# Kernel tuning notes

Hardware: AMD Instinct MI355X
Metric: run time of the kernel (lower is better)

The kernel has to match this reference:

```python
import jax, jax.numpy as jnp
import numpy as np
from jax import lax
from jax.scipy.special import logsumexp

NUM_STATES = 32
INPUT_SIZE = 128
HIDDEN = 256
LN_EPS = 1e-5


def setup_inputs() -> dict:
    key = jax.random.key(0)
    ks = jax.random.split(key, 8)
    B, T = 32, 8192
    x = jax.random.normal(ks[0], (B, T, INPUT_SIZE), dtype=jnp.float32)
    # parameters (match torch defaults: initial_logits=zeros, transition_logits=2*I)
    initial_logits = jnp.zeros((NUM_STATES,), jnp.float32)
    transition_logits = 2.0 * jnp.eye(NUM_STATES, dtype=jnp.float32)
    W1 = jax.random.normal(ks[1], (INPUT_SIZE, HIDDEN), jnp.float32) / np.sqrt(INPUT_SIZE)
    b1 = jnp.zeros((HIDDEN,), jnp.float32)
    ln_g = jnp.ones((HIDDEN,), jnp.float32)
    ln_b = jnp.zeros((HIDDEN,), jnp.float32)
    W2 = jax.random.normal(ks[2], (HIDDEN, HIDDEN), jnp.float32) / np.sqrt(HIDDEN)
    b2 = jnp.zeros((HIDDEN,), jnp.float32)
    W3 = jax.random.normal(ks[3], (HIDDEN, NUM_STATES), jnp.float32) / np.sqrt(HIDDEN)
    b3 = jnp.zeros((NUM_STATES,), jnp.float32)
    return {"x": x, "initial_logits": initial_logits, "transition_logits": transition_logits,
            "W1": W1, "b1": b1, "ln_g": ln_g, "ln_b": ln_b, "W2": W2, "b2": b2, "W3": W3, "b3": b3}


def _emission_logprobs(x, W1, b1, ln_g, ln_b, W2, b2, W3, b3):
    h = x @ W1 + b1                                   # (B,T,H)
    mu = h.mean(-1, keepdims=True)
    var = ((h - mu) ** 2).mean(-1, keepdims=True)
    h = (h - mu) * lax.rsqrt(var + LN_EPS) * ln_g + ln_b
    h = jax.nn.gelu(h, approximate=False)             # torch nn.GELU default = exact
    h = jax.nn.gelu(h @ W2 + b2, approximate=False)
    logits = h @ W3 + b3                              # (B,T,S)  (dropout inactive at eval)
    return jax.nn.log_softmax(logits, axis=-1)


def reference(x, initial_logits, transition_logits, W1, b1, ln_g, ln_b, W2, b2, W3, b3):
    emissions = _emission_logprobs(x, W1, b1, ln_g, ln_b, W2, b2, W3, b3)  # (B,T,S)
    B = x.shape[0]
    trans = jax.nn.softmax(transition_logits, axis=-1)
    log_trans = jnp.log(trans + 1e-10)                               # (S,S)
    log_init = jnp.log(jax.nn.softmax(initial_logits) + 1e-10)       # (S,)

    alpha0 = log_init[None, :] + emissions[:, 0, :]                  # (B,S)
    em_rest = jnp.swapaxes(emissions[:, 1:, :], 0, 1)                # (T-1,B,S)

    # --- forward algorithm (log-sum-exp semiring scan over time) ---
    def fwd_step(alpha, em_t):
        a = em_t + logsumexp(alpha[:, :, None] + log_trans[None, :, :], axis=1)
        return a, a
    _, alphas_rest = lax.scan(fwd_step, alpha0, em_rest)             # (T-1,B,S)
    alphas = jnp.concatenate([alpha0[:, None, :], jnp.swapaxes(alphas_rest, 0, 1)], axis=1)  # (B,T,S)
    log_likelihood = logsumexp(alphas[:, -1, :], axis=-1)            # (B,)
    state_probs = jax.nn.softmax(alphas, axis=-1)

    # --- Viterbi (max-plus semiring scan + backtrace) ---
    def vit_step(vit, em_t):
        scores = vit[:, :, None] + log_trans[None, :, :]             # (B,S,S)
        return scores.max(axis=1) + em_t, scores.argmax(axis=1)
    vit_last, bps = lax.scan(vit_step, alpha0, em_rest)              # bps: (T-1,B,S) int32
    path_score = vit_last.max(axis=-1)
    last_state = vit_last.argmax(axis=-1)                            # (B,)
    bidx = jnp.arange(B)

    def bt_step(state, bp):
        prev = bp[bidx, state]
        return prev, prev
    _, path_prefix = lax.scan(bt_step, last_state, bps, reverse=True)  # (T-1,B)
    best_path = jnp.concatenate([jnp.swapaxes(path_prefix, 0, 1), last_state[:, None]], axis=1)  # (B,T)

    return (emissions, state_probs, log_likelihood, trans, best_path, path_score)
```

## Files before the change

kernel.cpp:

```cpp
#include <hip/hip_runtime.h>
#include <cstdint>
#include <cstddef>

#define TT 8192
#define SS 32

__device__ __forceinline__ float rsum32(float v){
    v += __shfl_xor(v,16); v += __shfl_xor(v,8); v += __shfl_xor(v,4);
    v += __shfl_xor(v,2);  v += __shfl_xor(v,1); return v;
}
__device__ __forceinline__ float rmax32(float v){
    v = fmaxf(v,__shfl_xor(v,16)); v = fmaxf(v,__shfl_xor(v,8)); v = fmaxf(v,__shfl_xor(v,4));
    v = fmaxf(v,__shfl_xor(v,2));  v = fmaxf(v,__shfl_xor(v,1)); return v;
}
__device__ __forceinline__ void lds_read32(const float* p, float* d){
    #pragma unroll
    for (int k=0;k<8;k++){
        float4 v = ((const float4*)p)[k];
        d[4*k+0]=v.x; d[4*k+1]=v.y; d[4*k+2]=v.z; d[4*k+3]=v.w;
    }
}
__device__ __forceinline__ float arr_sum32(const float* a){
    float s0=0.f,s1=0.f,s2=0.f,s3=0.f;
    #pragma unroll
    for (int k=0;k<32;k+=4){ s0+=a[k]; s1+=a[k+1]; s2+=a[k+2]; s3+=a[k+3]; }
    return (s0+s1)+(s2+s3);
}
__device__ __forceinline__ float arr_max32(const float* a){
    float s0=a[0],s1=a[1],s2=a[2],s3=a[3];
    #pragma unroll
    for (int k=4;k<32;k+=4){ s0=fmaxf(s0,a[k]); s1=fmaxf(s1,a[k+1]); s2=fmaxf(s2,a[k+2]); s3=fmaxf(s3,a[k+3]); }
    return fmaxf(fmaxf(s0,s1),fmaxf(s2,s3));
}
__device__ __forceinline__ float dot32(const float* a, const float* b){
    float s0=0.f,s1=0.f,s2=0.f,s3=0.f;
    #pragma unroll
    for (int k=0;k<32;k+=4){
        s0=fmaf(a[k],b[k],s0); s1=fmaf(a[k+1],b[k+1],s1);
        s2=fmaf(a[k+2],b[k+2],s2); s3=fmaf(a[k+3],b[k+3],s3);
    }
    return (s0+s1)+(s2+s3);
}
__device__ __forceinline__ float gelu_exact(float v){
    return 0.5f*v*(1.0f + erff(v*0.70710678118654752440f));
}

__global__ __launch_bounds__(1024) void hmm_prep(
    const float* __restrict__ il, const float* __restrict__ tl,
    float* __restrict__ trans, float* __restrict__ lt, float* __restrict__ li,
    float* __restrict__ LL, float* __restrict__ PS)
{
    const int tid = threadIdx.x;
    const int c = tid & 31;
    const float v = tl[tid];
    const float m = rmax32(v);
    const float e = expf(v - m);
    const float ssum = rsum32(e);
    const float t = e / ssum;
    trans[tid] = t;
    lt[tid] = logf(t + 1e-10f);
    if (tid < 32){
        const float iv = il[c];
        const float m2 = rmax32(iv);
        const float e2 = expf(iv - m2);
        const float s2 = rsum32(e2);
        li[c] = logf(e2/s2 + 1e-10f);
        LL[c] = 0.f;
        PS[c] = 0.f;
    }
}

__global__ __launch_bounds__(256) void hmm_mlp(
    const float* __restrict__ x,
    const float* __restrict__ W1, const float* __restrict__ b1,
    const float* __restrict__ lng, const float* __restrict__ lnb,
    const float* __restrict__ W2, const float* __restrict__ b2,
    const float* __restrict__ W3, const float* __restrict__ b3,
    float* __restrict__ em_out)
{
    __shared__ float smem[16384];
    float* h1s = smem;
    float* xs  = smem + 8192;
    float* h2s = smem + 8192;

    const int tid = threadIdx.x;
    const int row0 = blockIdx.x << 5;

    {
        const float4* xg = (const float4*)(x + (size_t)row0*128);
        float4* xs4 = (float4*)xs;
        #pragma unroll
        for (int l=0;l<4;l++) xs4[tid + (l<<8)] = xg[tid + (l<<8)];
    }
    __syncthreads();

    const int tc_ = tid & 31;
    const int ty  = tid >> 5;
    const int c0  = tc_ << 3;
    const int r0g = ty << 2;

    float acc[4][8];
    #pragma unroll
    for (int i=0;i<4;i++){
        #pragma unroll
        for (int j=0;j<8;j++) acc[i][j]=0.f;
    }

    {
        const float4* W14 = (const float4*)W1;
        #pragma unroll 2
        for (int k4=0;k4<32;k4++){
            float xv[4][4];
            #pragma unroll
            for (int i=0;i<4;i++){
                float4 t = *(const float4*)&xs[(r0g+i)*128 + (k4<<2)];
                xv[i][0]=t.x; xv[i][1]=t.y; xv[i][2]=t.z; xv[i][3]=t.w;
            }
            #pragma unroll
            for (int kk=0;kk<4;kk++){
                const int k = (k4<<2)+kk;
                const float4 wa = W14[k*64 + (tc_<<1)];
                const float4 wb = W14[k*64 + (tc_<<1) + 1];
                const float w[8] = {wa.x,wa.y,wa.z,wa.w,wb.x,wb.y,wb.z,wb.w};
                #pragma unroll
                for (int i=0;i<4;i++){
                    #pragma unroll
                    for (int j=0;j<8;j++) acc[i][j] = fmaf(xv[i][kk], w[j], acc[i][j]);
                }
            }
        }
    }

    {
        float4 ta = *(const float4*)&b1[c0];  float4 tb = *(const float4*)&b1[c0+4];
        const float bb[8] = {ta.x,ta.y,ta.z,ta.w,tb.x,tb.y,tb.z,tb.w};
        ta = *(const float4*)&lng[c0]; tb = *(const float4*)&lng[c0+4];
        const float gg[8] = {ta.x,ta.y,ta.z,ta.w,tb.x,tb.y,tb.z,tb.w};
        ta = *(const float4*)&lnb[c0]; tb = *(const float4*)&lnb[c0+4];
        const float be[8] = {ta.x,ta.y,ta.z,ta.w,tb.x,tb.y,tb.z,tb.w};
        #pragma unroll
        for (int i=0;i<4;i++){
            float sm=0.f;
            #pragma unroll
            for (int j=0;j<8;j++){ float v = acc[i][j]+bb[j]; acc[i][j]=v; sm+=v; }
            float sq=0.f;
            #pragma unroll
            for (int j=0;j<8;j++) sq = fmaf(acc[i][j],acc[i][j],sq);
            sm = rsum32(sm); sq = rsum32(sq);
            const float mu = sm*(1.f/256.f);
            const float var = sq*(1.f/256.f) - mu*mu;
            const float rstd = rsqrtf(var + 1e-5f);
            #pragma unroll
            for (int j=0;j<8;j++){
                float v = (acc[i][j]-mu)*rstd*gg[j] + be[j];
                acc[i][j] = gelu_exact(v);
            }
            float4 s0 = make_float4(acc[i][0],acc[i][1],acc[i][2],acc[i][3]);
            float4 s1 = make_float4(acc[i][4],acc[i][5],acc[i][6],acc[i][7]);
            *(float4*)&h1s[(r0g+i)*256 + c0]     = s0;
            *(float4*)&h1s[(r0g+i)*256 + c0 + 4] = s1;
        }
    }
    __syncthreads();

    #pragma unroll
    for (int i=0;i<4;i++){
        #pragma unroll
        for (int j=0;j<8;j++) acc[i][j]=0.f;
    }
    {
        const float4* W24 = (const float4*)W2;
        #pragma unroll 2
        for (int k4=0;k4<64;k4++){
            float xv[4][4];
            #pragma unroll
            for (int i=0;i<4;i++){
                float4 t = *(const float4*)&h1s[(r0g+i)*256 + (k4<<2)];
                xv[i][0]=t.x; xv[i][1]=t.y; xv[i][2]=t.z; xv[i][3]=t.w;
            }
            #pragma unroll
            for (int kk=0;kk<4;kk++){
                const int k = (k4<<2)+kk;
                const float4 wa = W24[k*64 + (tc_<<1)];
                const float4 wb = W24[k*64 + (tc_<<1) + 1];
                const float w[8] = {wa.x,wa.y,wa.z,wa.w,wb.x,wb.y,wb.z,wb.w};
                #pragma unroll
                for (int i=0;i<4;i++){
                    #pragma unroll
                    for (int j=0;j<8;j++) acc[i][j] = fmaf(xv[i][kk], w[j], acc[i][j]);
                }
            }
        }
    }
    {
        float4 ta = *(const float4*)&b2[c0];  float4 tb = *(const float4*)&b2[c0+4];
        const float bb[8] = {ta.x,ta.y,ta.z,ta.w,tb.x,tb.y,tb.z,tb.w};
        #pragma unroll
        for (int i=0;i<4;i++){
            const int r = r0g + i;
            const int sw = (r & 7) << 2;
            #pragma unroll
            for (int j=0;j<8;j++) acc[i][j] = gelu_exact(acc[i][j]+bb[j]);
            float4 s0 = make_float4(acc[i][0],acc[i][1],acc[i][2],acc[i][3]);
            float4 s1 = make_float4(acc[i][4],acc[i][5],acc[i][6],acc[i][7]);
            *(float4*)&h2s[r*256 + (c0 ^ sw)]       = s0;
            *(float4*)&h2s[r*256 + ((c0+4) ^ sw)]   = s1;
        }
    }
    __syncthreads();

    {
        const int r3 = tid >> 3;
        const int cg = tid & 7;
        const int sw3 = (r3 & 7) << 2;
        float a3[4] = {0.f,0.f,0.f,0.f};
        const float4* W34 = (const float4*)W3;
        #pragma unroll 2
        for (int k4=0;k4<64;k4++){
            float4 hv = *(const float4*)&h2s[r3*256 + ((k4<<2) ^ sw3)];
            const float h[4] = {hv.x,hv.y,hv.z,hv.w};
            #pragma unroll
            for (int kk=0;kk<4;kk++){
                float4 w = W34[((k4<<2)+kk)*8 + cg];
                a3[0]=fmaf(h[kk],w.x,a3[0]); a3[1]=fmaf(h[kk],w.y,a3[1]);
                a3[2]=fmaf(h[kk],w.z,a3[2]); a3[3]=fmaf(h[kk],w.w,a3[3]);
            }
        }
        float4 b3v = ((const float4*)b3)[cg];
        a3[0]+=b3v.x; a3[1]+=b3v.y; a3[2]+=b3v.z; a3[3]+=b3v.w;
        float m = fmaxf(fmaxf(a3[0],a3[1]),fmaxf(a3[2],a3[3]));
        m = fmaxf(m,__shfl_xor(m,4)); m = fmaxf(m,__shfl_xor(m,2)); m = fmaxf(m,__shfl_xor(m,1));
        float se = expf(a3[0]-m)+expf(a3[1]-m)+expf(a3[2]-m)+expf(a3[3]-m);
        se += __shfl_xor(se,4); se += __shfl_xor(se,2); se += __shfl_xor(se,1);
        const float lz = m + logf(se);
        float4 o = make_float4(a3[0]-lz, a3[1]-lz, a3[2]-lz, a3[3]-lz);
        *(float4*)&em_out[((size_t)(row0+r3))*32 + (cg<<2)] = o;
    }
}

__global__ __launch_bounds__(256) void hmm_fwd(
    const float* __restrict__ em, const float* __restrict__ trans,
    const float* __restrict__ li, float* __restrict__ sp, float* __restrict__ LL)
{
    __shared__ float Ab[8][32];
    const int lane = threadIdx.x & 63;
    const int s = lane & 31;
    const int ci = ((threadIdx.x >> 6) << 1) | (lane >> 5);
    const int cid = (blockIdx.x << 3) + ci;
    const int b = cid >> 7;
    const int c = cid & 127;
    const int t0 = c << 6;

    float tc[32];
    #pragma unroll
    for (int k=0;k<32;k++) tc[k] = trans[(k<<5) + s];
    float* A = Ab[ci];
    const float* emb = em + (size_t)b*(TT*SS);
    const float li_s = li[s];

    A[s] = 0.03125f;
    asm volatile("s_waitcnt lgkmcnt(0)" ::: "memory");
    __builtin_amdgcn_wave_barrier();

    float sig = 0.f;
    float araw_prev = 0.f;

    const int tws = t0 - 64;
    float pe[8];
    #pragma unroll
    for (int j=0;j<8;j++){ int tt = tws + j; tt = tt < 0 ? 0 : tt; pe[j] = emb[(tt<<5) + s]; }

    #pragma unroll 1
    for (int g=0; g<8; g++){
        float ce[8];
        #pragma unroll
        for (int j=0;j<8;j++) ce[j] = pe[j];
        #pragma unroll
        for (int j=0;j<8;j++){ int tt = tws + ((g+1)<<3) + j; tt = tt < 0 ? 0 : tt; pe[j] = emb[(tt<<5) + s]; }
        #pragma unroll
        for (int j=0;j<8;j++){
            float Av[32];
            lds_read32(A, Av);
            const float sum = arr_sum32(Av);
            const float val = dot32(Av, tc);
            const float rs = 1.0f / sum;
            const float e = __expf(ce[j]);
            const float araw = val * rs * e;
            __builtin_amdgcn_wave_barrier();
            A[s] = araw;
            asm volatile("s_waitcnt lgkmcnt(0)" ::: "memory");
            __builtin_amdgcn_wave_barrier();
        }
    }

    #pragma unroll 1
    for (int g=0; g<8; g++){
        float ce[8];
        #pragma unroll
        for (int j=0;j<8;j++) ce[j] = pe[j];
        #pragma unroll
        for (int j=0;j<8;j++){ int tt = t0 + ((g+1)<<3) + j; tt = tt > (TT-1) ? (TT-1) : tt; pe[j] = emb[(tt<<5) + s]; }
        #pragma unroll
        for (int j=0;j<8;j++){
            const int i = (g<<3) + j;
            const int t = t0 + i;
            float Av[32];
            lds_read32(A, Av);
            const float sum = arr_sum32(Av);
            const float val = dot32(Av, tc);
            const float rs = 1.0f / sum;
            if (i > 0){
                sp[((size_t)b*TT + (t-1))*SS + s] = araw_prev * rs;
                sig += __logf(sum);
            }
            const float e = __expf(ce[j]);
            float araw = val * rs * e;
            if (c == 0 && i == 0) araw = __expf(li_s) * e;
            __builtin_amdgcn_wave_barrier();
            A[s] = araw;
            asm volatile("s_waitcnt lgkmcnt(0)" ::: "memory");
            __builtin_amdgcn_wave_barrier();
            araw_prev = araw;
        }
    }
    {
        float Av[32];
        lds_read32(A, Av);
        const float sum = arr_sum32(Av);
        const float rs = 1.0f / sum;
        sp[((size_t)b*TT + (t0+63))*SS + s] = araw_prev * rs;
        sig += __logf(sum);
    }
    if (s == 0) atomicAdd(&LL[b], sig);
}

__global__ __launch_bounds__(256) void hmm_vit(
    const float* __restrict__ em, const float* __restrict__ lt,
    const float* __restrict__ li, unsigned char* __restrict__ bps,
    float* __restrict__ PS, int* __restrict__ last_state)
{
    __shared__ float Vb[8][32];
    const int lane = threadIdx.x & 63;
    const int s = lane & 31;
    const int ci = ((threadIdx.x >> 6) << 1) | (lane >> 5);
    const int cid = (blockIdx.x << 3) + ci;
    const int b = cid >> 7;
    const int c = cid & 127;
    const int t0 = c << 6;

    float ltc[32];
    #pragma unroll
    for (int k=0;k<32;k++) ltc[k] = lt[(k<<5) + s];
    float* V = Vb[ci];
    const float* emb = em + (size_t)b*(TT*SS);
    const float li_s = li[s];

    V[s] = 0.f;
    asm volatile("s_waitcnt lgkmcnt(0)" ::: "memory");
    __builtin_amdgcn_wave_barrier();

    float delta = 0.f;

    const int tws = t0 - 128;
    float pe[8];
    #pragma unroll
    for (int j=0;j<8;j++){ int tt = tws + j; tt = tt < 0 ? 0 : tt; pe[j] = emb[(tt<<5) + s]; }

    #pragma unroll 1
    for (int g=0; g<16; g++){
        float ce[8];
        #pragma unroll
        for (int j=0;j<8;j++) ce[j] = pe[j];
        #pragma unroll
        for (int j=0;j<8;j++){ int tt = tws + ((g+1)<<3) + j; tt = tt < 0 ? 0 : tt; pe[j] = emb[(tt<<5) + s]; }
        #pragma unroll
        for (int j=0;j<8;j++){
            float Vv[32];
            lds_read32(V, Vv);
            float b0=-3.0e38f,b1v=-3.0e38f,b2v=-3.0e38f,b3v=-3.0e38f;
            #pragma unroll
            for (int k=0;k<32;k+=4){
                b0  = fmaxf(b0,  Vv[k]+ltc[k]);
                b1v = fmaxf(b1v, Vv[k+1]+ltc[k+1]);
                b2v = fmaxf(b2v, Vv[k+2]+ltc[k+2]);
                b3v = fmaxf(b3v, Vv[k+3]+ltc[k+3]);
            }
            float v = fmaxf(fmaxf(b0,b1v),fmaxf(b2v,b3v)) + ce[j];
            if (j == 7) v -= arr_max32(Vv);
            __builtin_amdgcn_wave_barrier();
            V[s] = v;
            asm volatile("s_waitcnt lgkmcnt(0)" ::: "memory");
            __builtin_amdgcn_wave_barrier();
        }
    }
    {
        float Vv[32];
        lds_read32(V, Vv);
        const float mm = arr_max32(Vv);
        __builtin_amdgcn_wave_barrier();
        V[s] = Vv[s] - mm;
        asm volatile("s_waitcnt lgkmcnt(0)" ::: "memory");
        __builtin_amdgcn_wave_barrier();
    }

    #pragma unroll 1
    for (int g=0; g<8; g++){
        float ce[8];
        #pragma unroll
        for (int j=0;j<8;j++) ce[j] = pe[j];
        #pragma unroll
        for (int j=0;j<8;j++){ int tt = t0 + ((g+1)<<3) + j; tt = tt > (TT-1) ? (TT-1) : tt; pe[j] = emb[(tt<<5) + s]; }
        #pragma unroll
        for (int j=0;j<8;j++){
            const int i = (g<<3) + j;
            const int t = t0 + i;
            float Vv[32];
            lds_read32(V, Vv);
            float B0=Vv[0]+ltc[0], B1=Vv[1]+ltc[1], B2=Vv[2]+ltc[2], B3=Vv[3]+ltc[3];
            int I0=0,I1=1,I2=2,I3=3;
            #pragma unroll
            for (int k=4;k<32;k+=4){
                float q0=Vv[k]+ltc[k];     if (q0>B0){B0=q0;I0=k;}
                float q1=Vv[k+1]+ltc[k+1]; if (q1>B1){B1=q1;I1=k+1;}
                float q2=Vv[k+2]+ltc[k+2]; if (q2>B2){B2=q2;I2=k+2;}
                float q3=Vv[k+3]+ltc[k+3]; if (q3>B3){B3=q3;I3=k+3;}
            }
            float best = B0; int bi = I0;
            if (B1>best || (B1==best && I1<bi)){best=B1;bi=I1;}
            if (B2>best || (B2==best && I2<bi)){best=B2;bi=I2;}
            if (B3>best || (B3==best && I3<bi)){best=B3;bi=I3;}
            float mmc = 0.f;
            if (j == 0){ mmc = arr_max32(Vv); delta += mmc; }
            float v;
            if (c == 0 && i == 0){
                v = li_s + ce[j];
            } else {
                v = best + ce[j] - mmc;
                bps[((size_t)b*TT + t)*SS + s] = (unsigned char)bi;
            }
            __builtin_amdgcn_wave_barrier();
            V[s] = v;
            asm volatile("s_waitcnt lgkmcnt(0)" ::: "memory");
            __builtin_amdgcn_wave_barrier();
        }
    }
    {
        float Vv[32];
        lds_read32(V, Vv);
        const float mm = arr_max32(Vv);
        delta += mm;
        if (c == 127){
            float best = Vv[0]; int bi = 0;
            #pragma unroll
            for (int k=1;k<32;k++){ if (Vv[k] > best){ best = Vv[k]; bi = k; } }
            if (s == 0) last_state[b] = bi;
        }
        if (s == 0) atomicAdd(&PS[b], delta);
    }
}

__global__ __launch_bounds__(64) void hmm_btc(
    const unsigned char* __restrict__ bps, unsigned char* __restrict__ pos,
    unsigned char* __restrict__ gmap)
{
    __shared__ unsigned char bp[8192];
    const int b = blockIdx.x >> 5;
    const int cb = blockIdx.x & 31;
    const int tbase = cb << 8;
    {
        const uint4* src = (const uint4*)(bps + ((size_t)b*TT + tbase)*SS);
        uint4* dst = (uint4*)bp;
        #pragma unroll
        for (int l=0;l<8;l++) dst[threadIdx.x + (l<<6)] = src[threadIdx.x + (l<<6)];
    }
    __syncthreads();
    if (threadIdx.x < 32){
        int cur = threadIdx.x;
        unsigned char* pc = pos + (((size_t)b<<5) + cb)*8192;
        #pragma unroll 1
        for (int t=255; t>=0; t--){
            pc[(t<<5) + threadIdx.x] = (unsigned char)cur;
            if ((tbase + t) >= 1) cur = bp[(t<<5) + cur];
        }
        gmap[(((b<<5) + cb)<<5) + threadIdx.x] = (unsigned char)cur;
    }
}

__global__ __launch_bounds__(256) void hmm_btb(
    const unsigned char* __restrict__ gmap, const int* __restrict__ last_state,
    unsigned char* __restrict__ e_tab)
{
    __shared__ unsigned char gl[32768];
    #pragma unroll
    for (int l=0;l<8;l++) ((uint4*)gl)[threadIdx.x + (l<<8)] = ((const uint4*)gmap)[threadIdx.x + (l<<8)];
    __syncthreads();
    if (threadIdx.x < 32){
        const int b = threadIdx.x;
        int s = last_state[b];
        #pragma unroll 1
        for (int cb=31; cb>=1; cb--){
            e_tab[(b<<5)+cb] = (unsigned char)s;
            s = gl[(((b<<5)+cb)<<5) + s];
        }
        e_tab[b<<5] = (unsigned char)s;
    }
}

__global__ __launch_bounds__(256) void hmm_btf(
    const unsigned char* __restrict__ pos, const unsigned char* __restrict__ e_tab,
    float* __restrict__ path)
{
    const int i = blockIdx.x*256 + threadIdx.x;
    const int b = i >> 13;
    const int t = i & (TT-1);
    const int cb = t >> 8;
    const int e = e_tab[(b<<5) + cb];
    const unsigned char v = pos[((((size_t)b<<5) + cb)<<13) + ((t & 255)<<5) + e];
    path[i] = (float)v;
}

extern "C" void kernel_launch(void* const* d_in, const int* in_sizes, int n_in,
                              void* d_out, int out_size, void* d_ws, size_t ws_size,
                              hipStream_t stream)
{
    const float* x   = (const float*)d_in[0];
    const float* il  = (const float*)d_in[1];
    const float* tl  = (const float*)d_in[2];
    const float* W1  = (const float*)d_in[3];
    const float* b1  = (const float*)d_in[4];
    const float* lng = (const float*)d_in[5];
    const float* lnb = (const float*)d_in[6];
    const float* W2  = (const float*)d_in[7];
    const float* b2  = (const float*)d_in[8];
    const float* W3  = (const float*)d_in[9];
    const float* b3  = (const float*)d_in[10];

    float* out   = (float*)d_out;
    float* em    = out;
    float* sp    = out + 8388608;
    float* LL    = out + 16777216;
    float* trans = out + 16777248;
    float* path  = out + 16778272;
    float* PS    = out + 17040416;

    char* wsb = (char*)d_ws;
    float* lt            = (float*)(wsb);
    float* li            = (float*)(wsb + 4096);
    int* last_state      = (int*)(wsb + 4224);
    unsigned char* e_tab = (unsigned char*)(wsb + 4352);
    unsigned char* bps   = (unsigned char*)(wsb + 8192);
    unsigned char* pos   = (unsigned char*)(wsb + 8192 + 8388608);
    unsigned char* gmap  = (unsigned char*)(wsb + 8192 + 16777216);

    hmm_prep<<<1, 1024, 0, stream>>>(il, tl, trans, lt, li, LL, PS);
    hmm_mlp<<<8192, 256, 0, stream>>>(x, W1, b1, lng, lnb, W2, b2, W3, b3, em);
    hmm_fwd<<<512, 256, 0, stream>>>(em, trans, li, sp, LL);
    hmm_vit<<<512, 256, 0, stream>>>(em, lt, li, bps, PS, last_state);
    hmm_btc<<<1024, 64, 0, stream>>>(bps, pos, gmap);
    hmm_btb<<<1, 256, 0, stream>>>(gmap, last_state, e_tab);
    hmm_btf<<<1024, 256, 0, stream>>>(pos, e_tab, path);
}
```

Baseline: 1.434 ms.

## Restructure MLP kernel so each wavefront owns rows, removing block barriers

The emission MLP is remapped so each 64-lane wavefront owns 8 rows and each lane owns 4 output columns. The x tile is no longer staged in LDS: x is read directly from global memory through a wave-uniform pointer, and the hidden activations reuse a single 32 KB LDS buffer in place. Since every wavefront only reads rows it wrote itself, all block-wide __syncthreads are dropped. LDS use is halved and launch_bounds asks for 5 blocks per CU to raise occupancy, at the cost of reading x from global per k-step and a tighter register budget.

```diff
diff --git a/kernel.cpp b/kernel.cpp
--- a/kernel.cpp
+++ b/kernel.cpp
@@ -12,6 +12,10 @@
 __device__ __forceinline__ float rmax32(float v){
     v = fmaxf(v,__shfl_xor(v,16)); v = fmaxf(v,__shfl_xor(v,8)); v = fmaxf(v,__shfl_xor(v,4));
     v = fmaxf(v,__shfl_xor(v,2));  v = fmaxf(v,__shfl_xor(v,1)); return v;
+}
+__device__ __forceinline__ float rsum64(float v){
+    v += __shfl_xor(v,32); v += __shfl_xor(v,16); v += __shfl_xor(v,8);
+    v += __shfl_xor(v,4);  v += __shfl_xor(v,2);  v += __shfl_xor(v,1); return v;
 }
 __device__ __forceinline__ void lds_read32(const float* p, float* d){
     #pragma unroll
@@ -70,7 +74,7 @@
     }
 }
 
-__global__ __launch_bounds__(256) void hmm_mlp(
+__global__ __launch_bounds__(256, 5) void hmm_mlp(
     const float* __restrict__ x,
     const float* __restrict__ W1, const float* __restrict__ b1,
     const float* __restrict__ lng, const float* __restrict__ lnb,
@@ -78,155 +82,114 @@
     const float* __restrict__ W3, const float* __restrict__ b3,
     float* __restrict__ em_out)
 {
-    __shared__ float smem[16384];
-    float* h1s = smem;
-    float* xs  = smem + 8192;
-    float* h2s = smem + 8192;
-
-    const int tid = threadIdx.x;
+    __shared__ float hbuf[8192];
+    const int tid  = threadIdx.x;
+    const int lane = tid & 63;
+    const int wv   = tid >> 6;
     const int row0 = blockIdx.x << 5;
-
-    {
-        const float4* xg = (const float4*)(x + (size_t)row0*128);
-        float4* xs4 = (float4*)xs;
-        #pragma unroll
-        for (int l=0;l<4;l++) xs4[tid + (l<<8)] = xg[tid + (l<<8)];
-    }
-    __syncthreads();
-
-    const int tc_ = tid & 31;
-    const int ty  = tid >> 5;
-    const int c0  = tc_ << 3;
-    const int r0g = ty << 2;
-
-    float acc[4][8];
-    #pragma unroll
-    for (int i=0;i<4;i++){
-        #pragma unroll
-        for (int j=0;j<8;j++) acc[i][j]=0.f;
-    }
-
-    {
-        const float4* W14 = (const float4*)W1;
-        #pragma unroll 2
-        for (int k4=0;k4<32;k4++){
-            float xv[4][4];
-            #pragma unroll
-            for (int i=0;i<4;i++){
-                float4 t = *(const float4*)&xs[(r0g+i)*128 + (k4<<2)];
-                xv[i][0]=t.x; xv[i][1]=t.y; xv[i][2]=t.z; xv[i][3]=t.w;
-            }
-            #pragma unroll
-            for (int kk=0;kk<4;kk++){
-                const int k = (k4<<2)+kk;
-                const float4 wa = W14[k*64 + (tc_<<1)];
-                const float4 wb = W14[k*64 + (tc_<<1) + 1];
-                const float w[8] = {wa.x,wa.y,wa.z,wa.w,wb.x,wb.y,wb.z,wb.w};
-                #pragma unroll
-                for (int i=0;i<4;i++){
-                    #pragma unroll
-                    for (int j=0;j<8;j++) acc[i][j] = fmaf(xv[i][kk], w[j], acc[i][j]);
-                }
-            }
-        }
-    }
-
-    {
-        float4 ta = *(const float4*)&b1[c0];  float4 tb = *(const float4*)&b1[c0+4];
-        const float bb[8] = {ta.x,ta.y,ta.z,ta.w,tb.x,tb.y,tb.z,tb.w};
-        ta = *(const float4*)&lng[c0]; tb = *(const float4*)&lng[c0+4];
-        const float gg[8] = {ta.x,ta.y,ta.z,ta.w,tb.x,tb.y,tb.z,tb.w};
-        ta = *(const float4*)&lnb[c0]; tb = *(const float4*)&lnb[c0+4];
-        const float be[8] = {ta.x,ta.y,ta.z,ta.w,tb.x,tb.y,tb.z,tb.w};
-        #pragma unroll
-        for (int i=0;i<4;i++){
-            float sm=0.f;
-            #pragma unroll
-            for (int j=0;j<8;j++){ float v = acc[i][j]+bb[j]; acc[i][j]=v; sm+=v; }
-            float sq=0.f;
-            #pragma unroll
-            for (int j=0;j<8;j++) sq = fmaf(acc[i][j],acc[i][j],sq);
-            sm = rsum32(sm); sq = rsum32(sq);
-            const float mu = sm*(1.f/256.f);
-            const float var = sq*(1.f/256.f) - mu*mu;
+    const int r0   = wv << 3;
+    const int c0   = lane << 2;
+
+    const int r0u = __builtin_amdgcn_readfirstlane(r0);
+    const float* xw = x + ((size_t)(row0 + r0u) << 7);
+
+    float acc[8][4];
+    #pragma unroll
+    for (int i=0;i<8;i++){ acc[i][0]=0.f; acc[i][1]=0.f; acc[i][2]=0.f; acc[i][3]=0.f; }
+
+    #pragma unroll 2
+    for (int k4=0;k4<32;k4++){
+        const float4 w0 = *(const float4*)&W1[((k4<<2)+0)*256 + c0];
+        const float4 w1 = *(const float4*)&W1[((k4<<2)+1)*256 + c0];
+        const float4 w2 = *(const float4*)&W1[((k4<<2)+2)*256 + c0];
+        const float4 w3 = *(const float4*)&W1[((k4<<2)+3)*256 + c0];
+        #pragma unroll
+        for (int i=0;i<8;i++){
+            const float4 xv = *(const float4*)(xw + (i<<7) + (k4<<2));
+            acc[i][0]=fmaf(xv.x,w0.x,acc[i][0]); acc[i][1]=fmaf(xv.x,w0.y,acc[i][1]);
+            acc[i][2]=fmaf(xv.x,w0.z,acc[i][2]); acc[i][3]=fmaf(xv.x,w0.w,acc[i][3]);
+            acc[i][0]=fmaf(xv.y,w1.x,acc[i][0]); acc[i][1]=fmaf(xv.y,w1.y,acc[i][1]);
+            acc[i][2]=fmaf(xv.y,w1.z,acc[i][2]); acc[i][3]=fmaf(xv.y,w1.w,acc[i][3]);
+            acc[i][0]=fmaf(xv.z,w2.x,acc[i][0]); acc[i][1]=fmaf(xv.z,w2.y,acc[i][1]);
+            acc[i][2]=fmaf(xv.z,w2.z,acc[i][2]); acc[i][3]=fmaf(xv.z,w2.w,acc[i][3]);
+            acc[i][0]=fmaf(xv.w,w3.x,acc[i][0]); acc[i][1]=fmaf(xv.w,w3.y,acc[i][1]);
+            acc[i][2]=fmaf(xv.w,w3.z,acc[i][2]); acc[i][3]=fmaf(xv.w,w3.w,acc[i][3]);
+        }
+    }
+
+    {
+        const float4 bb = *(const float4*)&b1[c0];
+        const float4 gg = *(const float4*)&lng[c0];
+        const float4 be = *(const float4*)&lnb[c0];
+        #pragma unroll
+        for (int i=0;i<8;i++){
+            float a0=acc[i][0]+bb.x, a1=acc[i][1]+bb.y, a2=acc[i][2]+bb.z, a3=acc[i][3]+bb.w;
+            float sm = (a0+a1)+(a2+a3);
+            float sq = fmaf(a0,a0,fmaf(a1,a1,fmaf(a2,a2,a3*a3)));
+            sm = rsum64(sm); sq = rsum64(sq);
+            const float mu   = sm*(1.f/256.f);
+            const float var  = sq*(1.f/256.f) - mu*mu;
             const float rstd = rsqrtf(var + 1e-5f);
-            #pragma unroll
-            for (int j=0;j<8;j++){
-                float v = (acc[i][j]-mu)*rstd*gg[j] + be[j];
-                acc[i][j] = gelu_exact(v);
-            }
-            float4 s0 = make_float4(acc[i][0],acc[i][1],acc[i][2],acc[i][3]);
-            float4 s1 = make_float4(acc[i][4],acc[i][5],acc[i][6],acc[i][7]);
-            *(float4*)&h1s[(r0g+i)*256 + c0]     = s0;
-            *(float4*)&h1s[(r0g+i)*256 + c0 + 4] = s1;
-        }
-    }
-    __syncthreads();
-
-    #pragma unroll
-    for (int i=0;i<4;i++){
-        #pragma unroll
-        for (int j=0;j<8;j++) acc[i][j]=0.f;
-    }
-    {
-        const float4* W24 = (const float4*)W2;
-        #pragma unroll 2
-        for (int k4=0;k4<64;k4++){
-            float xv[4][4];
-            #pragma unroll
-            for (int i=0;i<4;i++){
-                float4 t = *(const float4*)&h1s[(r0g+i)*256 + (k4<<2)];
-                xv[i][0]=t.x; xv[i][1]=t.y; xv[i][2]=t.z; xv[i][3]=t.w;
-            }
-            #pragma unroll
-            for (int kk=0;kk<4;kk++){
-                const int k = (k4<<2)+kk;
-                const float4 wa = W24[k*64 + (tc_<<1)];
-                const float4 wb = W24[k*64 + (tc_<<1) + 1];
-                const float w[8] = {wa.x,wa.y,wa.z,wa.w,wb.x,wb.y,wb.z,wb.w};
-                #pragma unroll
-                for (int i=0;i<4;i++){
-                    #pragma unroll
-                    for (int j=0;j<8;j++) acc[i][j] = fmaf(xv[i][kk], w[j], acc[i][j]);
-                }
-            }
-        }
-    }
-    {
-        float4 ta = *(const float4*)&b2[c0];  float4 tb = *(const float4*)&b2[c0+4];
-        const float bb[8] = {ta.x,ta.y,ta.z,ta.w,tb.x,tb.y,tb.z,tb.w};
-        #pragma unroll
-        for (int i=0;i<4;i++){
-            const int r = r0g + i;
-            const int sw = (r & 7) << 2;
-            #pragma unroll
-            for (int j=0;j<8;j++) acc[i][j] = gelu_exact(acc[i][j]+bb[j]);
-            float4 s0 = make_float4(acc[i][0],acc[i][1],acc[i][2],acc[i][3]);
-            float4 s1 = make_float4(acc[i][4],acc[i][5],acc[i][6],acc[i][7]);
-            *(float4*)&h2s[r*256 + (c0 ^ sw)]       = s0;
-            *(float4*)&h2s[r*256 + ((c0+4) ^ sw)]   = s1;
-        }
-    }
-    __syncthreads();
-
-    {
-        const int r3 = tid >> 3;
-        const int cg = tid & 7;
+            a0 = gelu_exact((a0-mu)*rstd*gg.x + be.x);
+            a1 = gelu_exact((a1-mu)*rstd*gg.y + be.y);
+            a2 = gelu_exact((a2-mu)*rstd*gg.z + be.z);
+            a3 = gelu_exact((a3-mu)*rstd*gg.w + be.w);
+            *(float4*)&hbuf[(r0+i)*256 + c0] = make_float4(a0,a1,a2,a3);
+        }
+    }
+
+    #pragma unroll
+    for (int i=0;i<8;i++){ acc[i][0]=0.f; acc[i][1]=0.f; acc[i][2]=0.f; acc[i][3]=0.f; }
+    #pragma unroll 2
+    for (int k4=0;k4<64;k4++){
+        const float4 w0 = *(const float4*)&W2[((k4<<2)+0)*256 + c0];
+        const float4 w1 = *(const float4*)&W2[((k4<<2)+1)*256 + c0];
+        const float4 w2 = *(const float4*)&W2[((k4<<2)+2)*256 + c0];
+        const float4 w3 = *(const float4*)&W2[((k4<<2)+3)*256 + c0];
+        #pragma unroll
+        for (int i=0;i<8;i++){
+            const float4 hv = *(const float4*)&hbuf[(r0+i)*256 + (k4<<2)];
+            acc[i][0]=fmaf(hv.x,w0.x,acc[i][0]); acc[i][1]=fmaf(hv.x,w0.y,acc[i][1]);
+            acc[i][2]=fmaf(hv.x,w0.z,acc[i][2]); acc[i][3]=fmaf(hv.x,w0.w,acc[i][3]);
+            acc[i][0]=fmaf(hv.y,w1.x,acc[i][0]); acc[i][1]=fmaf(hv.y,w1.y,acc[i][1]);
+            acc[i][2]=fmaf(hv.y,w1.z,acc[i][2]); acc[i][3]=fmaf(hv.y,w1.w,acc[i][3]);
+            acc[i][0]=fmaf(hv.z,w2.x,acc[i][0]); acc[i][1]=fmaf(hv.z,w2.y,acc[i][1]);
+            acc[i][2]=fmaf(hv.z,w2.z,acc[i][2]); acc[i][3]=fmaf(hv.z,w2.w,acc[i][3]);
+            acc[i][0]=fmaf(hv.w,w3.x,acc[i][0]); acc[i][1]=fmaf(hv.w,w3.y,acc[i][1]);
+            acc[i][2]=fmaf(hv.w,w3.z,acc[i][2]); acc[i][3]=fmaf(hv.w,w3.w,acc[i][3]);
+        }
+    }
+    {
+        const float4 bv = *(const float4*)&b2[c0];
+        #pragma unroll
+        for (int i=0;i<8;i++){
+            const int r = r0+i;
+            const float a0 = gelu_exact(acc[i][0]+bv.x);
+            const float a1 = gelu_exact(acc[i][1]+bv.y);
+            const float a2 = gelu_exact(acc[i][2]+bv.z);
+            const float a3 = gelu_exact(acc[i][3]+bv.w);
+            *(float4*)&hbuf[r*256 + (c0 ^ ((r&7)<<2))] = make_float4(a0,a1,a2,a3);
+        }
+    }
+
+    {
+        const int r3  = tid >> 3;
+        const int cg  = tid & 7;
         const int sw3 = (r3 & 7) << 2;
         float a3[4] = {0.f,0.f,0.f,0.f};
         const float4* W34 = (const float4*)W3;
         #pragma unroll 2
         for (int k4=0;k4<64;k4++){
-            float4 hv = *(const float4*)&h2s[r3*256 + ((k4<<2) ^ sw3)];
+            const float4 hv = *(const float4*)&hbuf[r3*256 + ((k4<<2) ^ sw3)];
             const float h[4] = {hv.x,hv.y,hv.z,hv.w};
             #pragma unroll
             for (int kk=0;kk<4;kk++){
-                float4 w = W34[((k4<<2)+kk)*8 + cg];
+                const float4 w = W34[((k4<<2)+kk)*8 + cg];
                 a3[0]=fmaf(h[kk],w.x,a3[0]); a3[1]=fmaf(h[kk],w.y,a3[1]);
                 a3[2]=fmaf(h[kk],w.z,a3[2]); a3[3]=fmaf(h[kk],w.w,a3[3]);
             }
         }
-        float4 b3v = ((const float4*)b3)[cg];
+        const float4 b3v = ((const float4*)b3)[cg];
         a3[0]+=b3v.x; a3[1]+=b3v.y; a3[2]+=b3v.z; a3[3]+=b3v.w;
         float m = fmaxf(fmaxf(a3[0],a3[1]),fmaxf(a3[2],a3[3]));
         m = fmaxf(m,__shfl_xor(m,4)); m = fmaxf(m,__shfl_xor(m,2)); m = fmaxf(m,__shfl_xor(m,1));
```

Result: no change. 1.432 ms (-0.2%).
